# Kernel optimization log

Hardware: AMD Instinct MI355X
Metric: run time of the kernel (lower is better)

The kernel has to match this reference:

```python
import jax, jax.numpy as jnp
import numpy as np

D = 96  # voxel grid extent; two stride-2 stages -> 48 -> 24


def _dense(coords, feats, C):
    # scatter sparse points onto a dense [D,D,D,C] grid + occupancy mask
    i, j, k = coords[:, 0], coords[:, 1], coords[:, 2]
    grid = jnp.zeros((D, D, D, C), feats.dtype).at[i, j, k].add(feats)
    occ = jnp.zeros((D, D, D, 1), feats.dtype).at[i, j, k].set(1.0)
    return grid, occ


def _conv(x, W, b, stride, padding):
    # x: [D,H,W,Cin], W: [kd,kh,kw,Cin,Cout]
    y = jax.lax.conv_general_dilated(
        x[None], W, (stride,) * 3, padding,
        dimension_numbers=("NDHWC", "DHWIO", "NDHWC"))[0]
    return y + b


def _pool2(occ):
    # stride-2 kernel-2 sparse conv output coords == 2x2x2 maxpool of occupancy
    return jax.lax.reduce_window(occ, 0.0, jax.lax.max,
                                 (2, 2, 2, 1), (2, 2, 2, 1), "VALID")


def setup_inputs() -> dict:
    key = jax.random.key(0)
    ks = jax.random.split(key, 12)
    N = 120000
    coords = jax.random.randint(ks[0], (N, 3), 0, D, dtype=jnp.int32)
    feats = jax.random.normal(ks[1], (N, 8), dtype=jnp.float32)
    s = 0.05
    return {
        "coords": coords,
        "feats": feats,
        "W0": jax.random.normal(ks[2], (3, 3, 3, 8, 16), jnp.float32) * s,
        "b0": jax.random.normal(ks[3], (16,), jnp.float32) * s,
        "Wd0": jax.random.normal(ks[4], (2, 2, 2, 16, 32), jnp.float32) * s,
        "bd0": jax.random.normal(ks[5], (32,), jnp.float32) * s,
        "W1": jax.random.normal(ks[6], (3, 3, 3, 32, 32), jnp.float32) * s,
        "b1": jax.random.normal(ks[7], (32,), jnp.float32) * s,
        "Wd1": jax.random.normal(ks[8], (2, 2, 2, 32, 64), jnp.float32) * s,
        "bd1": jax.random.normal(ks[9], (64,), jnp.float32) * s,
        "W2": jax.random.normal(ks[10], (3, 3, 3, 64, 64), jnp.float32) * s,
        "b2": jax.random.normal(ks[11], (64,), jnp.float32) * s,
    }


def reference(coords, feats, W0, b0, Wd0, bd0, W1, b1, Wd1, bd1, W2, b2):
    x, occ = _dense(coords, feats, feats.shape[-1])
    relu = jax.nn.relu
    # conv0 (k3,s1) keeps coords -> mask with occ
    h = relu(_conv(x, W0, b0, 1, "SAME")) * occ
    occ0 = _pool2(occ)
    out0 = relu(_conv(h, Wd0, bd0, 2, "VALID")) * occ0  # [48,48,48,32]
    h1 = relu(_conv(out0, W1, b1, 1, "SAME")) * occ0
    occ1 = _pool2(occ0)
    out1 = relu(_conv(h1, Wd1, bd1, 2, "VALID")) * occ1  # [24,24,24,64]
    out2 = relu(_conv(out1, W2, b2, 1, "SAME")) * occ1   # [24,24,24,64]
    return (out2, out1, out0)
```

## Files before the change

kernel.cpp:

```cpp
#include <hip/hip_runtime.h>


constexpr int D0 = 96;

__global__ void scatter_kernel(const int* __restrict__ coords,
                               const float* __restrict__ feats,
                               float* __restrict__ x, float* __restrict__ occ,
                               int N) {
    int n = blockIdx.x * blockDim.x + threadIdx.x;
    if (n >= N) return;
    int i = coords[n * 3 + 0], j = coords[n * 3 + 1], k = coords[n * 3 + 2];
    int flat = (i * D0 + j) * D0 + k;
    const float4* f4 = reinterpret_cast<const float4*>(feats + (size_t)n * 8);
    float4 a = f4[0], b = f4[1];
    float* dst = x + (size_t)flat * 8;
    atomicAdd(dst + 0, a.x); atomicAdd(dst + 1, a.y);
    atomicAdd(dst + 2, a.z); atomicAdd(dst + 3, a.w);
    atomicAdd(dst + 4, b.x); atomicAdd(dst + 5, b.y);
    atomicAdd(dst + 6, b.z); atomicAdd(dst + 7, b.w);
    occ[flat] = 1.0f;
}

template <int GDO>
__global__ void pool_kernel(const float* __restrict__ occ_in,
                            float* __restrict__ occ_out) {
    int idx = blockIdx.x * blockDim.x + threadIdx.x;
    if (idx >= GDO * GDO * GDO) return;
    int x = idx % GDO, y = (idx / GDO) % GDO, z = idx / (GDO * GDO);
    constexpr int GDI = GDO * 2;
    float m = 0.f;
    #pragma unroll
    for (int dz = 0; dz < 2; dz++)
        #pragma unroll
        for (int dy = 0; dy < 2; dy++)
            #pragma unroll
            for (int dx = 0; dx < 2; dx++)
                m = fmaxf(m, occ_in[((z * 2 + dz) * GDI + y * 2 + dy) * GDI + x * 2 + dx]);
    occ_out[idx] = m;
}

template <int CIN, int COUT, int GD, int TX, int TY, int TZ, int CC, int COSPLIT>
__global__ __launch_bounds__(256) void conv3_kernel(
    const float* __restrict__ in, const float* __restrict__ W,
    const float* __restrict__ bias, const float* __restrict__ occ,
    float* __restrict__ out) {
    constexpr int HX = TX + 2, HY = TY + 2, HZ = TZ + 2;
    constexpr int NV = HX * HY * HZ;
    constexpr int VOX = TX * TY * TZ;
    constexpr int NG = 256 / VOX;
    constexpr int CO_PER = COUT / COSPLIT / NG;
    constexpr int NCH = CIN / CC;
    __shared__ float4 lds4[(CC / 4) * NV];

    const int t = threadIdx.x;
    constexpr int NBX = GD / TX;
    const int cs = blockIdx.x / NBX;
    const int bx = blockIdx.x % NBX;
    const int x0 = bx * TX, y0 = blockIdx.y * TY, z0 = blockIdx.z * TZ;
    const int v = t % VOX;
    const int g = t / VOX;
    const int tx = v % TX, ty = (v / TX) % TY, tz = v / (TX * TY);
    const int co_base = __builtin_amdgcn_readfirstlane((cs * NG + g) * CO_PER);

    float acc[CO_PER];
    #pragma unroll
    for (int i = 0; i < CO_PER; i++) acc[i] = 0.f;

    for (int ch = 0; ch < NCH; ++ch) {
        constexpr int T4 = NV * (CC / 4);
        for (int idx = t; idx < T4; idx += 256) {
            int c4 = idx % (CC / 4);
            int vox = idx / (CC / 4);
            int hx = vox % HX, hy = (vox / HX) % HY, hz = vox / (HX * HY);
            int gx = x0 + hx - 1, gy = y0 + hy - 1, gz = z0 + hz - 1;
            float4 val = make_float4(0.f, 0.f, 0.f, 0.f);
            if (gx >= 0 && gx < GD && gy >= 0 && gy < GD && gz >= 0 && gz < GD) {
                val = *reinterpret_cast<const float4*>(
                    in + (size_t)((gz * GD + gy) * GD + gx) * CIN + ch * CC + c4 * 4);
            }
            lds4[c4 * NV + vox] = val;
        }
        __syncthreads();
        #pragma unroll 1
        for (int tap = 0; tap < 27; ++tap) {
            int kx = tap % 3, ky = (tap / 3) % 3, kz = tap / 9;
            int vin = (tz + kz) * (HX * HY) + (ty + ky) * HX + (tx + kx);
            #pragma unroll
            for (int c4 = 0; c4 < CC / 4; ++c4) {
                float4 iv = lds4[c4 * NV + vin];
                const float* wp =
                    W + (size_t)(tap * CIN + ch * CC + c4 * 4) * COUT + co_base;
                #pragma unroll
                for (int o4 = 0; o4 < CO_PER / 4; ++o4) {
                    float4 w0 = *reinterpret_cast<const float4*>(wp + 0 * COUT + o4 * 4);
                    float4 w1 = *reinterpret_cast<const float4*>(wp + 1 * COUT + o4 * 4);
                    float4 w2 = *reinterpret_cast<const float4*>(wp + 2 * COUT + o4 * 4);
                    float4 w3 = *reinterpret_cast<const float4*>(wp + 3 * COUT + o4 * 4);
                    acc[o4 * 4 + 0] += iv.x * w0.x + iv.y * w1.x + iv.z * w2.x + iv.w * w3.x;
                    acc[o4 * 4 + 1] += iv.x * w0.y + iv.y * w1.y + iv.z * w2.y + iv.w * w3.y;
                    acc[o4 * 4 + 2] += iv.x * w0.z + iv.y * w1.z + iv.z * w2.z + iv.w * w3.z;
                    acc[o4 * 4 + 3] += iv.x * w0.w + iv.y * w1.w + iv.z * w2.w + iv.w * w3.w;
                }
            }
        }
        __syncthreads();
    }
    int oz = z0 + tz, oy = y0 + ty, ox = x0 + tx;
    int oflat = (oz * GD + oy) * GD + ox;
    float o = occ[oflat];
    float* op = out + (size_t)oflat * COUT + co_base;
    #pragma unroll
    for (int o4 = 0; o4 < CO_PER / 4; o4++) {
        float4 r;
        r.x = fmaxf(acc[o4 * 4 + 0] + bias[co_base + o4 * 4 + 0], 0.f) * o;
        r.y = fmaxf(acc[o4 * 4 + 1] + bias[co_base + o4 * 4 + 1], 0.f) * o;
        r.z = fmaxf(acc[o4 * 4 + 2] + bias[co_base + o4 * 4 + 2], 0.f) * o;
        r.w = fmaxf(acc[o4 * 4 + 3] + bias[co_base + o4 * 4 + 3], 0.f) * o;
        *reinterpret_cast<float4*>(op + o4 * 4) = r;
    }
}

template <int CIN, int COUT, int GDI, int CC>
__global__ __launch_bounds__(256) void convd_kernel(
    const float* __restrict__ in, const float* __restrict__ W,
    const float* __restrict__ bias, const float* __restrict__ occ,
    float* __restrict__ out) {
    constexpr int GDO = GDI / 2;
    constexpr int VOX = 64, NG = 4;
    constexpr int CO_PER = COUT / NG;
    constexpr int HX = 8, HY = 8, HZ = 8, NV = HX * HY * HZ;
    constexpr int NCH = CIN / CC;
    __shared__ float4 lds4[(CC / 4) * NV];

    const int t = threadIdx.x;
    const int x0 = blockIdx.x * 4, y0 = blockIdx.y * 4, z0 = blockIdx.z * 4;
    const int v = t % VOX;
    const int g = t / VOX;
    const int tx = v % 4, ty = (v / 4) % 4, tz = v / 16;
    const int co_base = __builtin_amdgcn_readfirstlane(g * CO_PER);

    float acc[CO_PER];
    #pragma unroll
    for (int i = 0; i < CO_PER; i++) acc[i] = 0.f;

    for (int ch = 0; ch < NCH; ++ch) {
        constexpr int T4 = NV * (CC / 4);
        for (int idx = t; idx < T4; idx += 256) {
            int c4 = idx % (CC / 4);
            int vox = idx / (CC / 4);
            int hx = vox % HX, hy = (vox / HX) % HY, hz = vox / (HX * HY);
            int gx = x0 * 2 + hx, gy = y0 * 2 + hy, gz = z0 * 2 + hz;
            lds4[c4 * NV + vox] = *reinterpret_cast<const float4*>(
                in + (size_t)((gz * GDI + gy) * GDI + gx) * CIN + ch * CC + c4 * 4);
        }
        __syncthreads();
        #pragma unroll 1
        for (int tap = 0; tap < 8; ++tap) {
            int kx = tap & 1, ky = (tap >> 1) & 1, kz = tap >> 2;
            int vin = (tz * 2 + kz) * (HX * HY) + (ty * 2 + ky) * HX + (tx * 2 + kx);
            #pragma unroll
            for (int c4 = 0; c4 < CC / 4; ++c4) {
                float4 iv = lds4[c4 * NV + vin];
                const float* wp =
                    W + (size_t)(tap * CIN + ch * CC + c4 * 4) * COUT + co_base;
                #pragma unroll
                for (int o4 = 0; o4 < CO_PER / 4; ++o4) {
                    float4 w0 = *reinterpret_cast<const float4*>(wp + 0 * COUT + o4 * 4);
                    float4 w1 = *reinterpret_cast<const float4*>(wp + 1 * COUT + o4 * 4);
                    float4 w2 = *reinterpret_cast<const float4*>(wp + 2 * COUT + o4 * 4);
                    float4 w3 = *reinterpret_cast<const float4*>(wp + 3 * COUT + o4 * 4);
                    acc[o4 * 4 + 0] += iv.x * w0.x + iv.y * w1.x + iv.z * w2.x + iv.w * w3.x;
                    acc[o4 * 4 + 1] += iv.x * w0.y + iv.y * w1.y + iv.z * w2.y + iv.w * w3.y;
                    acc[o4 * 4 + 2] += iv.x * w0.z + iv.y * w1.z + iv.z * w2.z + iv.w * w3.z;
                    acc[o4 * 4 + 3] += iv.x * w0.w + iv.y * w1.w + iv.z * w2.w + iv.w * w3.w;
                }
            }
        }
        __syncthreads();
    }
    int oz = z0 + tz, oy = y0 + ty, ox = x0 + tx;
    int oflat = (oz * GDO + oy) * GDO + ox;
    float o = occ[oflat];
    float* op = out + (size_t)oflat * COUT + co_base;
    #pragma unroll
    for (int o4 = 0; o4 < CO_PER / 4; o4++) {
        float4 r;
        r.x = fmaxf(acc[o4 * 4 + 0] + bias[co_base + o4 * 4 + 0], 0.f) * o;
        r.y = fmaxf(acc[o4 * 4 + 1] + bias[co_base + o4 * 4 + 1], 0.f) * o;
        r.z = fmaxf(acc[o4 * 4 + 2] + bias[co_base + o4 * 4 + 2], 0.f) * o;
        r.w = fmaxf(acc[o4 * 4 + 3] + bias[co_base + o4 * 4 + 3], 0.f) * o;
        *reinterpret_cast<float4*>(op + o4 * 4) = r;
    }
}

extern "C" void kernel_launch(void* const* d_in, const int* in_sizes, int n_in,
                              void* d_out, int out_size, void* d_ws, size_t ws_size,
                              hipStream_t stream) {
    const int* coords = (const int*)d_in[0];
    const float* feats = (const float*)d_in[1];
    const float* W0 = (const float*)d_in[2];
    const float* b0 = (const float*)d_in[3];
    const float* Wd0 = (const float*)d_in[4];
    const float* bd0 = (const float*)d_in[5];
    const float* W1 = (const float*)d_in[6];
    const float* b1 = (const float*)d_in[7];
    const float* Wd1 = (const float*)d_in[8];
    const float* bd1 = (const float*)d_in[9];
    const float* W2 = (const float*)d_in[10];
    const float* b2 = (const float*)d_in[11];
    const int N = in_sizes[0] / 3;

    float* ws = (float*)d_ws;
    float* x = ws;
    float* h1 = ws;
    float* occ = ws + 7077888;
    float* h = ws + 7962624;
    float* occ0 = ws + 22118400;
    float* occ1 = ws + 22228992;

    float* out = (float*)d_out;
    float* out2 = out;
    float* out1 = out + 884736;
    float* out0 = out + 1769472;

    hipMemsetAsync(x, 0, (size_t)(7077888 + 884736) * sizeof(float), stream);

    scatter_kernel<<<(N + 255) / 256, 256, 0, stream>>>(coords, feats, x, occ, N);
    pool_kernel<48><<<(110592 + 255) / 256, 256, 0, stream>>>(occ, occ0);
    pool_kernel<24><<<(13824 + 255) / 256, 256, 0, stream>>>(occ0, occ1);

    conv3_kernel<8, 16, 96, 8, 8, 4, 8, 1>
        <<<dim3(12, 12, 24), 256, 0, stream>>>(x, W0, b0, occ, h);
    convd_kernel<16, 32, 96, 16>
        <<<dim3(12, 12, 12), 256, 0, stream>>>(h, Wd0, bd0, occ0, out0);
    conv3_kernel<32, 32, 48, 4, 4, 4, 16, 1>
        <<<dim3(12, 12, 12), 256, 0, stream>>>(out0, W1, b1, occ0, h1);
    convd_kernel<32, 64, 48, 16>
        <<<dim3(6, 6, 6), 256, 0, stream>>>(h1, Wd1, bd1, occ1, out1);
    conv3_kernel<64, 64, 24, 4, 4, 4, 16, 2>
        <<<dim3(12, 6, 6), 256, 0, stream>>>(out1, W2, b2, occ1, out2);
}
```

Before: 551.7 us.

## Pad LDS tiles, remap voxel layout, and retile conv3 channel chunks

Pads each channel-quad plane in the LDS halo buffer to reduce bank conflicts. Adds an optional thread-to-voxel remap for the last conv, restructures the tap loop into kz/ky/kx nests with row offsets hoisted, and skips the trailing barrier. Retiles conv1 to 8x4x4 with all 32 channels per chunk and doubles the channel chunk for conv2. The larger chunks mean fewer reload/sync rounds, but they use more shared memory, which may lower occupancy.

```diff
diff --git a/kernel.cpp b/kernel.cpp
--- a/kernel.cpp
+++ b/kernel.cpp
@@ -39,27 +39,40 @@
     occ_out[idx] = m;
 }
 
-template <int CIN, int COUT, int GD, int TX, int TY, int TZ, int CC, int COSPLIT>
+template <int CIN, int COUT, int GD, int TX, int TY, int TZ, int CC, int COSPLIT,
+          bool REMAP>
 __global__ __launch_bounds__(256) void conv3_kernel(
     const float* __restrict__ in, const float* __restrict__ W,
     const float* __restrict__ bias, const float* __restrict__ occ,
     float* __restrict__ out) {
     constexpr int HX = TX + 2, HY = TY + 2, HZ = TZ + 2;
     constexpr int NV = HX * HY * HZ;
+    constexpr int Q = CC / 4;
+    constexpr int PADV = 8 / Q;
+    constexpr int NVp = NV + PADV;
     constexpr int VOX = TX * TY * TZ;
     constexpr int NG = 256 / VOX;
     constexpr int CO_PER = COUT / COSPLIT / NG;
     constexpr int NCH = CIN / CC;
-    __shared__ float4 lds4[(CC / 4) * NV];
+    __shared__ float4 lds4[Q * NVp];
 
     const int t = threadIdx.x;
     constexpr int NBX = GD / TX;
     const int cs = blockIdx.x / NBX;
     const int bx = blockIdx.x % NBX;
     const int x0 = bx * TX, y0 = blockIdx.y * TY, z0 = blockIdx.z * TZ;
-    const int v = t % VOX;
+    const int v = t & (VOX - 1);
     const int g = t / VOX;
-    const int tx = v % TX, ty = (v / TX) % TY, tz = v / (TX * TY);
+    int tx, ty, tz;
+    if (REMAP) {
+        tx = v & 3;
+        ty = (v >> 3) & 3;
+        tz = ((v >> 2) & 1) | (((v >> 5) & 1) << 1);
+    } else {
+        tx = v % TX;
+        ty = (v / TX) % TY;
+        tz = v / (TX * TY);
+    }
     const int co_base = __builtin_amdgcn_readfirstlane((cs * NG + g) * CO_PER);
 
     float acc[CO_PER];
@@ -67,10 +80,10 @@
     for (int i = 0; i < CO_PER; i++) acc[i] = 0.f;
 
     for (int ch = 0; ch < NCH; ++ch) {
-        constexpr int T4 = NV * (CC / 4);
+        constexpr int T4 = NV * Q;
         for (int idx = t; idx < T4; idx += 256) {
-            int c4 = idx % (CC / 4);
-            int vox = idx / (CC / 4);
+            int c4 = idx & (Q - 1);
+            int vox = idx / Q;
             int hx = vox % HX, hy = (vox / HX) % HY, hz = vox / (HX * HY);
             int gx = x0 + hx - 1, gy = y0 + hy - 1, gz = z0 + hz - 1;
             float4 val = make_float4(0.f, 0.f, 0.f, 0.f);
@@ -78,32 +91,39 @@
                 val = *reinterpret_cast<const float4*>(
                     in + (size_t)((gz * GD + gy) * GD + gx) * CIN + ch * CC + c4 * 4);
             }
-            lds4[c4 * NV + vox] = val;
+            lds4[c4 * NVp + vox] = val;
         }
         __syncthreads();
         #pragma unroll 1
-        for (int tap = 0; tap < 27; ++tap) {
-            int kx = tap % 3, ky = (tap / 3) % 3, kz = tap / 9;
-            int vin = (tz + kz) * (HX * HY) + (ty + ky) * HX + (tx + kx);
-            #pragma unroll
-            for (int c4 = 0; c4 < CC / 4; ++c4) {
-                float4 iv = lds4[c4 * NV + vin];
-                const float* wp =
-                    W + (size_t)(tap * CIN + ch * CC + c4 * 4) * COUT + co_base;
+        for (int kz = 0; kz < 3; ++kz) {
+            #pragma unroll 1
+            for (int ky = 0; ky < 3; ++ky) {
+                const int vrow = (tz + kz) * (HX * HY) + (ty + ky) * HX + tx;
                 #pragma unroll
-                for (int o4 = 0; o4 < CO_PER / 4; ++o4) {
-                    float4 w0 = *reinterpret_cast<const float4*>(wp + 0 * COUT + o4 * 4);
-                    float4 w1 = *reinterpret_cast<const float4*>(wp + 1 * COUT + o4 * 4);
-                    float4 w2 = *reinterpret_cast<const float4*>(wp + 2 * COUT + o4 * 4);
-                    float4 w3 = *reinterpret_cast<const float4*>(wp + 3 * COUT + o4 * 4);
-                    acc[o4 * 4 + 0] += iv.x * w0.x + iv.y * w1.x + iv.z * w2.x + iv.w * w3.x;
-                    acc[o4 * 4 + 1] += iv.x * w0.y + iv.y * w1.y + iv.z * w2.y + iv.w * w3.y;
-                    acc[o4 * 4 + 2] += iv.x * w0.z + iv.y * w1.z + iv.z * w2.z + iv.w * w3.z;
-                    acc[o4 * 4 + 3] += iv.x * w0.w + iv.y * w1.w + iv.z * w2.w + iv.w * w3.w;
+                for (int kx = 0; kx < 3; ++kx) {
+                    const int tap = (kz * 3 + ky) * 3 + kx;
+                    const int vin = vrow + kx;
+                    #pragma unroll
+                    for (int c4 = 0; c4 < Q; ++c4) {
+                        float4 iv = lds4[c4 * NVp + vin];
+                        const float* wp =
+                            W + (size_t)(tap * CIN + ch * CC + c4 * 4) * COUT + co_base;
+                        #pragma unroll
+                        for (int o4 = 0; o4 < CO_PER / 4; ++o4) {
+                            float4 w0 = *reinterpret_cast<const float4*>(wp + 0 * COUT + o4 * 4);
+                            float4 w1 = *reinterpret_cast<const float4*>(wp + 1 * COUT + o4 * 4);
+                            float4 w2 = *reinterpret_cast<const float4*>(wp + 2 * COUT + o4 * 4);
+                            float4 w3 = *reinterpret_cast<const float4*>(wp + 3 * COUT + o4 * 4);
+                            acc[o4 * 4 + 0] += iv.x * w0.x + iv.y * w1.x + iv.z * w2.x + iv.w * w3.x;
+                            acc[o4 * 4 + 1] += iv.x * w0.y + iv.y * w1.y + iv.z * w2.y + iv.w * w3.y;
+                            acc[o4 * 4 + 2] += iv.x * w0.z + iv.y * w1.z + iv.z * w2.z + iv.w * w3.z;
+                            acc[o4 * 4 + 3] += iv.x * w0.w + iv.y * w1.w + iv.z * w2.w + iv.w * w3.w;
+                        }
+                    }
                 }
             }
         }
-        __syncthreads();
+        if (ch + 1 < NCH) __syncthreads();
     }
     int oz = z0 + tz, oy = y0 + ty, ox = x0 + tx;
     int oflat = (oz * GD + oy) * GD + ox;
@@ -129,13 +149,15 @@
     constexpr int VOX = 64, NG = 4;
     constexpr int CO_PER = COUT / NG;
     constexpr int HX = 8, HY = 8, HZ = 8, NV = HX * HY * HZ;
+    constexpr int Q = CC / 4;
+    constexpr int NVp = NV + 8 / Q;
     constexpr int NCH = CIN / CC;
-    __shared__ float4 lds4[(CC / 4) * NV];
+    __shared__ float4 lds4[Q * NVp];
 
     const int t = threadIdx.x;
     const int x0 = blockIdx.x * 4, y0 = blockIdx.y * 4, z0 = blockIdx.z * 4;
-    const int v = t % VOX;
-    const int g = t / VOX;
+    const int v = t & 63;
+    const int g = t >> 6;
     const int tx = v % 4, ty = (v / 4) % 4, tz = v / 16;
     const int co_base = __builtin_amdgcn_readfirstlane(g * CO_PER);
 
@@ -144,39 +166,45 @@
     for (int i = 0; i < CO_PER; i++) acc[i] = 0.f;
 
     for (int ch = 0; ch < NCH; ++ch) {
-        constexpr int T4 = NV * (CC / 4);
+        constexpr int T4 = NV * Q;
         for (int idx = t; idx < T4; idx += 256) {
-            int c4 = idx % (CC / 4);
-            int vox = idx / (CC / 4);
+            int c4 = idx & (Q - 1);
+            int vox = idx / Q;
             int hx = vox % HX, hy = (vox / HX) % HY, hz = vox / (HX * HY);
             int gx = x0 * 2 + hx, gy = y0 * 2 + hy, gz = z0 * 2 + hz;
-            lds4[c4 * NV + vox] = *reinterpret_cast<const float4*>(
+            lds4[c4 * NVp + vox] = *reinterpret_cast<const float4*>(
                 in + (size_t)((gz * GDI + gy) * GDI + gx) * CIN + ch * CC + c4 * 4);
         }
         __syncthreads();
         #pragma unroll 1
-        for (int tap = 0; tap < 8; ++tap) {
-            int kx = tap & 1, ky = (tap >> 1) & 1, kz = tap >> 2;
-            int vin = (tz * 2 + kz) * (HX * HY) + (ty * 2 + ky) * HX + (tx * 2 + kx);
+        for (int kz = 0; kz < 2; ++kz) {
             #pragma unroll
-            for (int c4 = 0; c4 < CC / 4; ++c4) {
-                float4 iv = lds4[c4 * NV + vin];
-                const float* wp =
-                    W + (size_t)(tap * CIN + ch * CC + c4 * 4) * COUT + co_base;
+            for (int ky = 0; ky < 2; ++ky) {
                 #pragma unroll
-                for (int o4 = 0; o4 < CO_PER / 4; ++o4) {
-                    float4 w0 = *reinterpret_cast<const float4*>(wp + 0 * COUT + o4 * 4);
-                    float4 w1 = *reinterpret_cast<const float4*>(wp + 1 * COUT + o4 * 4);
-                    float4 w2 = *reinterpret_cast<const float4*>(wp + 2 * COUT + o4 * 4);
-                    float4 w3 = *reinterpret_cast<const float4*>(wp + 3 * COUT + o4 * 4);
-                    acc[o4 * 4 + 0] += iv.x * w0.x + iv.y * w1.x + iv.z * w2.x + iv.w * w3.x;
-                    acc[o4 * 4 + 1] += iv.x * w0.y + iv.y * w1.y + iv.z * w2.y + iv.w * w3.y;
-                    acc[o4 * 4 + 2] += iv.x * w0.z + iv.y * w1.z + iv.z * w2.z + iv.w * w3.z;
-                    acc[o4 * 4 + 3] += iv.x * w0.w + iv.y * w1.w + iv.z * w2.w + iv.w * w3.w;
+                for (int kx = 0; kx < 2; ++kx) {
+                    const int tap = kz * 4 + ky * 2 + kx;
+                    const int vin = (tz * 2 + kz) * (HX * HY) + (ty * 2 + ky) * HX + (tx * 2 + kx);
+                    #pragma unroll
+                    for (int c4 = 0; c4 < Q; ++c4) {
+                        float4 iv = lds4[c4 * NVp + vin];
+                        const float* wp =
+                            W + (size_t)(tap * CIN + ch * CC + c4 * 4) * COUT + co_base;
+                        #pragma unroll
+                        for (int o4 = 0; o4 < CO_PER / 4; ++o4) {
+                            float4 w0 = *reinterpret_cast<const float4*>(wp + 0 * COUT + o4 * 4);
+                            float4 w1 = *reinterpret_cast<const float4*>(wp + 1 * COUT + o4 * 4);
+                            float4 w2 = *reinterpret_cast<const float4*>(wp + 2 * COUT + o4 * 4);
+                            float4 w3 = *reinterpret_cast<const float4*>(wp + 3 * COUT + o4 * 4);
+                            acc[o4 * 4 + 0] += iv.x * w0.x + iv.y * w1.x + iv.z * w2.x + iv.w * w3.x;
+                            acc[o4 * 4 + 1] += iv.x * w0.y + iv.y * w1.y + iv.z * w2.y + iv.w * w3.y;
+                            acc[o4 * 4 + 2] += iv.x * w0.z + iv.y * w1.z + iv.z * w2.z + iv.w * w3.z;
+                            acc[o4 * 4 + 3] += iv.x * w0.w + iv.y * w1.w + iv.z * w2.w + iv.w * w3.w;
+                        }
+                    }
                 }
             }
         }
-        __syncthreads();
+        if (ch + 1 < NCH) __syncthreads();
     }
     int oz = z0 + tz, oy = y0 + ty, ox = x0 + tx;
     int oflat = (oz * GDO + oy) * GDO + ox;
@@ -229,14 +257,14 @@
     pool_kernel<48><<<(110592 + 255) / 256, 256, 0, stream>>>(occ, occ0);
     pool_kernel<24><<<(13824 + 255) / 256, 256, 0, stream>>>(occ0, occ1);
 
-    conv3_kernel<8, 16, 96, 8, 8, 4, 8, 1>
+    conv3_kernel<8, 16, 96, 8, 8, 4, 8, 1, false>
         <<<dim3(12, 12, 24), 256, 0, stream>>>(x, W0, b0, occ, h);
     convd_kernel<16, 32, 96, 16>
         <<<dim3(12, 12, 12), 256, 0, stream>>>(h, Wd0, bd0, occ0, out0);
-    conv3_kernel<32, 32, 48, 4, 4, 4, 16, 1>
-        <<<dim3(12, 12, 12), 256, 0, stream>>>(out0, W1, b1, occ0, h1);
+    conv3_kernel<32, 32, 48, 8, 4, 4, 32, 1, false>
+        <<<dim3(6, 12, 12), 256, 0, stream>>>(out0, W1, b1, occ0, h1);
     convd_kernel<32, 64, 48, 16>
         <<<dim3(6, 6, 6), 256, 0, stream>>>(h1, Wd1, bd1, occ1, out1);
-    conv3_kernel<64, 64, 24, 4, 4, 4, 16, 2>
+    conv3_kernel<64, 64, 24, 4, 4, 4, 32, 2, true>
         <<<dim3(12, 6, 6), 256, 0, stream>>>(out1, W2, b2, occ1, out2);
 }
```

Measured after the change: 808.1 us. +46.5%, slower.
